# Kernel optimization log

Hardware: AMD Instinct MI355X
Metric: run time of the kernel (lower is better)

## Reference

```python
import jax, jax.numpy as jnp
import numpy as np

N_NODES = 50000


def gcn_conv(x, W, b, src, dst, ew, n_nodes):
    """PyG GCNConv: out = D^{-1/2}(A + I)D^{-1/2} (x @ W) + b, A weighted by ew.

    Self loops (weight 1) are handled analytically instead of appending edges.
    """
    h = x @ W  # [N, out]
    # degree includes self-loop weight of 1
    deg = jax.ops.segment_sum(ew, dst, num_segments=n_nodes) + 1.0  # [N]
    dinv = jnp.where(deg > 0, jax.lax.rsqrt(deg), 0.0)
    norm = dinv[src] * ew * dinv[dst]  # [E]
    # message = norm * h[src], scatter-add to dst
    agg = jax.ops.segment_sum(h[src] * norm[:, None], dst, num_segments=n_nodes)
    # self-loop contribution: dinv[i] * 1 * dinv[i] * h[i]
    agg = agg + h * (dinv * dinv)[:, None]
    return agg + b


def setup_inputs() -> dict:
    key = jax.random.key(0)
    k = jax.random.split(key, 8)
    n, e, d_in, d_h = N_NODES, 600000, 128, 128
    x = jax.random.normal(k[0], (n, d_in), dtype=jnp.float32)
    edge_index = jax.random.randint(k[1], (2, e), 0, n, dtype=jnp.int64)
    edge_attr = jax.random.uniform(k[2], (e,), dtype=jnp.float32)
    s1 = 1.0 / np.sqrt(d_in)
    s2 = 1.0 / np.sqrt(d_h)
    W1 = jax.random.uniform(k[3], (d_in, d_h), jnp.float32, -s1, s1)
    b1 = jnp.zeros((d_h,), jnp.float32)
    W2 = jax.random.uniform(k[4], (d_h, d_h), jnp.float32, -s2, s2)
    b2 = jnp.zeros((d_h,), jnp.float32)
    return {"x": x, "edge_index": edge_index, "edge_attr": edge_attr,
            "W1": W1, "b1": b1, "W2": W2, "b2": b2}


def reference(x, edge_index, edge_attr, W1, b1, W2, b2):
    src, dst = edge_index[0], edge_index[1]
    h = gcn_conv(x, W1, b1, src, dst, edge_attr, N_NODES)
    h = jax.nn.relu(h)
    # dropout is identity in eval mode (deterministic reference)
    out = gcn_conv(h, W2, b2, src, dst, edge_attr, N_NODES)
    return out
```

## Files before the change

### kernel.cpp

```cpp
#include <hip/hip_runtime.h>
#include <stdint.h>

#define D 128
#define EPB 4096
#define CSZ 128

typedef __bf16 bf16x8 __attribute__((ext_vector_type(8)));
typedef float f32x4 __attribute__((ext_vector_type(4)));

__device__ inline float bf2f(unsigned short u) {
    return __uint_as_float((unsigned)u << 16);
}
__device__ inline unsigned short f2bf(float f) {
    unsigned u = __float_as_uint(f);
    return (unsigned short)((u + 0x7FFF + ((u >> 16) & 1)) >> 16);
}

struct Params {
    const float* x; const int* ei; const float* ew;
    const float* W1; const float* b1; const float* W2; const float* b2;
    float* out;
    int N, E, C, B1n, total, gb, gb2, hb16, sb;
    unsigned short *Wt1, *Wt2;
    unsigned int* bh; int* ebase; int* bsums;
    float* dinv; int* cnt; int* rowstart;
    int2* brec; int2* erec;
    unsigned short *Hbuf, *Abuf;
};


__device__ inline void dev_prep(int which, const Params& p) {
    const float* W = (which == 0) ? p.W1 : p.W2;
    unsigned short* Wt = (which == 0) ? p.Wt1 : p.Wt2;
    for (int i = threadIdx.x; i < 2048; i += 256) {
        int nn = i >> 4;
        int kc = (i & 15) << 3;
        ushort4 o0, o1;
        o0.x = f2bf(W[(kc + 0) * 128 + nn]); o0.y = f2bf(W[(kc + 1) * 128 + nn]);
        o0.z = f2bf(W[(kc + 2) * 128 + nn]); o0.w = f2bf(W[(kc + 3) * 128 + nn]);
        o1.x = f2bf(W[(kc + 4) * 128 + nn]); o1.y = f2bf(W[(kc + 5) * 128 + nn]);
        o1.z = f2bf(W[(kc + 6) * 128 + nn]); o1.w = f2bf(W[(kc + 7) * 128 + nn]);
        *(ushort4*)(Wt + nn * 128 + kc) = o0;
        *(ushort4*)(Wt + nn * 128 + kc + 4) = o1;
    }
}

__device__ inline void dev_hist(int b, const Params& p, unsigned int* hist) {
    for (int i = threadIdx.x; i < p.C; i += 256) hist[i] = 0;
    __syncthreads();
    const int base = b * EPB + threadIdx.x;
#pragma unroll
    for (int k = 0; k < EPB / 256; ++k) {
        int e = base + k * 256;
        if (e < p.E) atomicAdd(&hist[((unsigned)p.ei[p.E + e]) >> 7], 1u);
    }
    __syncthreads();
    for (int i = threadIdx.x; i < p.C; i += 256) p.bh[(size_t)b * p.C + i] = hist[i];
}

__device__ inline void dev_scanA(int blk, const Params& p, int* tmp) {
    const int tid = threadIdx.x;
    const int i = blk * 256 + tid;
    int v = 0;
    if (i < p.total) {
        int c = i / p.B1n;
        int b = i - c * p.B1n;
        v = (int)p.bh[(size_t)b * p.C + c];
    }
    tmp[tid] = v;
    __syncthreads();
    for (int off = 1; off < 256; off <<= 1) {
        int t = (tid >= off) ? tmp[tid - off] : 0;
        __syncthreads();
        tmp[tid] += t;
        __syncthreads();
    }
    if (i < p.total) p.ebase[i] = tmp[tid] - v;
    if (tid == 255) p.bsums[blk] = tmp[255];
}

__device__ inline void block_pref(const Params& p, int* spref) {
    const int tid = threadIdx.x;
    int v = (tid < p.sb) ? p.bsums[tid] : 0;
    spref[tid] = v;
    __syncthreads();
    for (int off = 1; off < 256; off <<= 1) {
        int t = (tid >= off) ? spref[tid - off] : 0;
        __syncthreads();
        spref[tid] += t;
        __syncthreads();
    }
    int incl = spref[tid];
    __syncthreads();
    spref[tid] = incl - v;
    __syncthreads();
}

__device__ inline void dev_scat(int b, const Params& p, unsigned int* cur, const int* spref) {
    for (int i = threadIdx.x; i < p.C; i += 256) cur[i] = 0;
    __syncthreads();
    const int base = b * EPB + threadIdx.x;
#pragma unroll
    for (int k = 0; k < EPB / 256; ++k) {
        int e = base + k * 256;
        if (e < p.E) {
            int s = p.ei[e];
            unsigned d = (unsigned)p.ei[p.E + e];
            float w = p.ew[e];
            int c = d >> 7;
            unsigned r = atomicAdd(&cur[c], 1u);
            int idx = c * p.B1n + b;
            int pos = p.ebase[idx] + spref[idx >> 8] + (int)r;
            p.brec[pos] = make_int2((int)((d << 16) | (unsigned)s), __float_as_int(w));
        }
    }
}

__device__ inline void dev_cbuild(int c, const Params& p, unsigned int* a, const int* spref) {
    unsigned int* hcnt = a;
    unsigned int* hdeg = a + CSZ;
    unsigned int* lsc  = a + 2 * CSZ;
    unsigned int* curs = a + 3 * CSZ;
    const int tid = threadIdx.x;
    const int i0 = c * p.B1n;
    const int cs = p.ebase[i0] + spref[i0 >> 8];
    int ce;
    if (c + 1 < p.C) {
        const int i1 = (c + 1) * p.B1n;
        ce = p.ebase[i1] + spref[i1 >> 8];
    } else {
        ce = p.E;
    }
    if (tid < CSZ) { hcnt[tid] = 0; hdeg[tid] = 0; }
    __syncthreads();
    for (int i = cs + tid; i < ce; i += 256) {
        int2 r = p.brec[i];
        int local = (int)(((unsigned)r.x) >> 16) & (CSZ - 1);
        atomicAdd(&hcnt[local], 1u);
        atomicAdd(&hdeg[local], (unsigned)(__int_as_float(r.y) * 16777216.0f));
    }
    __syncthreads();
    if (tid < CSZ) lsc[tid] = hcnt[tid];
    __syncthreads();
    for (int off = 1; off < CSZ; off <<= 1) {
        unsigned t = (tid < CSZ && tid >= off) ? lsc[tid - off] : 0u;
        __syncthreads();
        if (tid < CSZ) lsc[tid] += t;
        __syncthreads();
    }
    if (tid < CSZ) {
        unsigned excl = lsc[tid] - hcnt[tid];
        curs[tid] = excl;
        int node = c * CSZ + tid;
        if (node < p.N) {
            p.rowstart[node] = cs + (int)excl;
            p.cnt[node] = (int)hcnt[tid];
            float deg = 1.0f + (float)hdeg[tid] * (1.0f / 16777216.0f);
            p.dinv[node] = rsqrtf(deg);
        }
    }
    __syncthreads();
    for (int i = cs + tid; i < ce; i += 256) {
        int2 r = p.brec[i];
        int local = (int)(((unsigned)r.x) >> 16) & (CSZ - 1);
        unsigned rk = atomicAdd(&curs[local], 1u);
        p.erec[cs + (int)rk] = make_int2(r.x & 0xFFFF, r.y);
    }
}

template <bool IN_BF16>
__device__ inline void mfma_body(unsigned short* sE,
                                 const void* __restrict__ Xv,
                                 const unsigned short* __restrict__ Wt,
                                 unsigned short* __restrict__ H, int n, int blk) {
    const int tid = threadIdx.x;
    const int row0 = blk * 64;
    const int lane = tid & 63;
    const int wv = tid >> 6;
    const int qm = lane & 15;
    const int quad = lane >> 4;

    const int arow = row0 + wv * 16 + qm;
    const int ar = (arow < n) ? arow : (n - 1);

    f32x4 acc[8];
#pragma unroll
    for (int i = 0; i < 8; ++i) acc[i] = (f32x4){0.f, 0.f, 0.f, 0.f};

#pragma unroll
    for (int kb = 0; kb < 4; ++kb) {
        const int koff = kb * 32 + quad * 8;
        bf16x8 a;
        if (IN_BF16) {
            a = *(const bf16x8*)((const unsigned short*)Xv + (size_t)ar * 128 + koff);
        } else {
            const float* Xf = (const float*)Xv + (size_t)ar * 128 + koff;
            float4 v0 = *(const float4*)(Xf);
            float4 v1 = *(const float4*)(Xf + 4);
            union { bf16x8 v; ushort4 u[2]; } cv;
            cv.u[0].x = f2bf(v0.x); cv.u[0].y = f2bf(v0.y);
            cv.u[0].z = f2bf(v0.z); cv.u[0].w = f2bf(v0.w);
            cv.u[1].x = f2bf(v1.x); cv.u[1].y = f2bf(v1.y);
            cv.u[1].z = f2bf(v1.z); cv.u[1].w = f2bf(v1.w);
            a = cv.v;
        }
#pragma unroll
        for (int n0 = 0; n0 < 8; ++n0) {
            bf16x8 b = *(const bf16x8*)(Wt + (n0 * 16 + qm) * 128 + koff);
            acc[n0] = __builtin_amdgcn_mfma_f32_16x16x32_bf16(a, b, acc[n0], 0, 0, 0);
        }
    }

#pragma unroll
    for (int n0 = 0; n0 < 8; ++n0)
#pragma unroll
        for (int r = 0; r < 4; ++r)
            sE[(wv * 16 + quad * 4 + r) * 136 + n0 * 16 + qm] = f2bf(acc[n0][r]);
    __syncthreads();

    const int row_in = lane >> 2;
    const int c0 = (lane & 3) * 4;
    const int grow = row0 + wv * 16 + row_in;
    if (grow < n) {
#pragma unroll
        for (int j = 0; j < 4; ++j)
            *(int4*)(H + (size_t)grow * 128 + (c0 + j) * 8) =
                *(const int4*)(&sE[(wv * 16 + row_in) * 136 + (c0 + j) * 8]);
    }
}

__device__ inline void gather1_node16(const Params& p, unsigned short* dst, int node, int lane) {
    const int4* __restrict__ H16 = (const int4*)p.Hbuf;
    union U8 { int4 v; unsigned short u[8]; };
    if (node < p.N) {
        const int start = p.rowstart[node];
        const int m = p.cnt[node];
        const float di = p.dinv[node];
        U8 s; s.v = H16[(size_t)node * 16 + lane];
        float acc[8];
#pragma unroll
        for (int q = 0; q < 8; ++q) acc[q] = di * bf2f(s.u[q]);

        const int2* __restrict__ er = p.erec + start;
        int j = 0;
        for (; j + 4 <= m; j += 4) {
            int2 e0 = er[j], e1 = er[j + 1], e2 = er[j + 2], e3 = er[j + 3];
            U8 v0, v1, v2, v3;
            v0.v = H16[(size_t)e0.x * 16 + lane];
            v1.v = H16[(size_t)e1.x * 16 + lane];
            v2.v = H16[(size_t)e2.x * 16 + lane];
            v3.v = H16[(size_t)e3.x * 16 + lane];
            float w0 = p.dinv[e0.x] * __int_as_float(e0.y);
            float w1 = p.dinv[e1.x] * __int_as_float(e1.y);
            float w2 = p.dinv[e2.x] * __int_as_float(e2.y);
            float w3 = p.dinv[e3.x] * __int_as_float(e3.y);
#pragma unroll
            for (int q = 0; q < 8; ++q)
                acc[q] += w0 * bf2f(v0.u[q]) + w1 * bf2f(v1.u[q]) +
                          w2 * bf2f(v2.u[q]) + w3 * bf2f(v3.u[q]);
        }
        for (; j < m; ++j) {
            int2 e0 = er[j];
            U8 v0; v0.v = H16[(size_t)e0.x * 16 + lane];
            float w0 = p.dinv[e0.x] * __int_as_float(e0.y);
#pragma unroll
            for (int q = 0; q < 8; ++q) acc[q] += w0 * bf2f(v0.u[q]);
        }
        const float4 b0 = *(const float4*)(p.b1 + lane * 8);
        const float4 b1v = *(const float4*)(p.b1 + lane * 8 + 4);
        const float bb[8] = {b0.x, b0.y, b0.z, b0.w, b1v.x, b1v.y, b1v.z, b1v.w};
        U8 o;
#pragma unroll
        for (int q = 0; q < 8; ++q) o.u[q] = f2bf(fmaxf(bb[q] + di * acc[q], 0.f));
        *(int4*)dst = o.v;
    } else {
        *(int4*)dst = (int4){0, 0, 0, 0};
    }
}

__device__ inline void gather2_body16(const Params& p, const int4* __restrict__ H16,
                                      const float* __restrict__ bias,
                                      float4* __restrict__ OUT, int g) {
    const int lane = threadIdx.x & 15;
    const int node = g * 16 + (threadIdx.x >> 4);
    if (node >= p.N) return;
    const int start = p.rowstart[node];
    const int m = p.cnt[node];
    const float di = p.dinv[node];

    union U8 { int4 v; unsigned short u[8]; };
    U8 s; s.v = H16[(size_t)node * 16 + lane];
    float acc[8];
#pragma unroll
    for (int q = 0; q < 8; ++q) acc[q] = bf2f(s.u[q]);

    const int2* __restrict__ er = p.erec + start;
    int j = 0;
    for (; j + 4 <= m; j += 4) {
        int2 e0 = er[j], e1 = er[j + 1], e2 = er[j + 2], e3 = er[j + 3];
        U8 v0, v1, v2, v3;
        v0.v = H16[(size_t)e0.x * 16 + lane];
        v1.v = H16[(size_t)e1.x * 16 + lane];
        v2.v = H16[(size_t)e2.x * 16 + lane];
        v3.v = H16[(size_t)e3.x * 16 + lane];
        float w0 = __int_as_float(e0.y), w1 = __int_as_float(e1.y);
        float w2 = __int_as_float(e2.y), w3 = __int_as_float(e3.y);
#pragma unroll
        for (int q = 0; q < 8; ++q)
            acc[q] += w0 * bf2f(v0.u[q]) + w1 * bf2f(v1.u[q]) +
                      w2 * bf2f(v2.u[q]) + w3 * bf2f(v3.u[q]);
    }
    for (; j < m; ++j) {
        int2 e0 = er[j];
        U8 v0; v0.v = H16[(size_t)e0.x * 16 + lane];
        float w0 = __int_as_float(e0.y);
#pragma unroll
        for (int q = 0; q < 8; ++q) acc[q] += w0 * bf2f(v0.u[q]);
    }

    const float4 b0 = *(const float4*)(bias + lane * 8);
    const float4 b1v = *(const float4*)(bias + lane * 8 + 4);
    float4 f0, f1;
    f0.x = b0.x + di * acc[0]; f0.y = b0.y + di * acc[1];
    f0.z = b0.z + di * acc[2]; f0.w = b0.w + di * acc[3];
    f1.x = b1v.x + di * acc[4]; f1.y = b1v.y + di * acc[5];
    f1.z = b1v.z + di * acc[6]; f1.w = b1v.w + di * acc[7];
    OUT[(size_t)node * 32 + lane * 2] = f0;
    OUT[(size_t)node * 32 + lane * 2 + 1] = f1;
}

__global__ __launch_bounds__(256, 4) void k_f0(Params p) {
    __shared__ __align__(16) unsigned int hist[512];
    if (blockIdx.x < 2) dev_prep(blockIdx.x, p);
    else dev_hist(blockIdx.x - 2, p, hist);
}
__global__ __launch_bounds__(256, 4) void k_f1(Params p) {
    __shared__ __align__(16) char arena[64 * 136 * 2];
    if ((int)blockIdx.x < p.gb) mfma_body<false>((unsigned short*)arena, (const void*)p.x, p.Wt1, p.Hbuf, p.N, blockIdx.x);
    else dev_scanA(blockIdx.x - p.gb, p, (int*)arena);
}
__global__ __launch_bounds__(256) void k_f3(Params p) {
    __shared__ unsigned int cur[512];
    __shared__ int spref[256];
    block_pref(p, spref);
    dev_scat(blockIdx.x, p, cur, spref);
}
__global__ __launch_bounds__(256) void k_f4(Params p) {
    __shared__ unsigned int a[4 * CSZ];
    __shared__ int spref[256];
    block_pref(p, spref);
    dev_cbuild(blockIdx.x, p, a, spref);
}
__global__ __launch_bounds__(256, 4) void k_g5(Params p) {
    __shared__ __align__(16) unsigned short sA[32 * 136];
    __shared__ __align__(16) unsigned short sE[32 * 136];
    const int row0 = blockIdx.x * 32;
    const int tid = threadIdx.x;

    const int lane16 = tid & 15;
    const int grp16 = tid >> 4;
#pragma unroll
    for (int pass = 0; pass < 2; ++pass) {
        const int local = pass * 16 + grp16;
        gather1_node16(p, sA + local * 136 + lane16 * 8, row0 + local, lane16);
    }
    __syncthreads();

    const int lane = tid & 63;
    const int wv = tid >> 6;
    const int qm = lane & 15;
    const int quad = lane >> 4;
    const int rh = wv & 1;
    const int ch = wv >> 1;

    f32x4 acc[4];
#pragma unroll
    for (int i = 0; i < 4; ++i) acc[i] = (f32x4){0.f, 0.f, 0.f, 0.f};

#pragma unroll
    for (int kb = 0; kb < 4; ++kb) {
        const int koff = kb * 32 + quad * 8;
        bf16x8 a = *(const bf16x8*)(sA + (rh * 16 + qm) * 136 + koff);
#pragma unroll
        for (int n0 = 0; n0 < 4; ++n0) {
            bf16x8 b = *(const bf16x8*)(p.Wt2 + ((ch * 4 + n0) * 16 + qm) * 128 + koff);
            acc[n0] = __builtin_amdgcn_mfma_f32_16x16x32_bf16(a, b, acc[n0], 0, 0, 0);
        }
    }

    const int crow = rh * 16 + quad * 4;
    float di[4];
#pragma unroll
    for (int r = 0; r < 4; ++r) {
        int rr = row0 + crow + r;
        int rc = (rr < p.N) ? rr : (p.N - 1);
        di[r] = p.dinv[rc];
    }

#pragma unroll
    for (int n0 = 0; n0 < 4; ++n0)
#pragma unroll
        for (int r = 0; r < 4; ++r)
            sE[(crow + r) * 136 + ch * 64 + n0 * 16 + qm] = f2bf(acc[n0][r] * di[r]);
    __syncthreads();

    const int row_in = tid >> 3;
    const int c0 = (tid & 7) * 2;
    const int grow = row0 + row_in;
    if (grow < p.N) {
        *(int4*)(p.Abuf + (size_t)grow * 128 + (c0 + 0) * 8) =
            *(const int4*)(&sE[row_in * 136 + (c0 + 0) * 8]);
        *(int4*)(p.Abuf + (size_t)grow * 128 + (c0 + 1) * 8) =
            *(const int4*)(&sE[row_in * 136 + (c0 + 1) * 8]);
    }
}
__global__ __launch_bounds__(256) void k_g6(Params p) {
    gather2_body16(p, (const int4*)p.Abuf, p.b2, (float4*)p.out, blockIdx.x);
}

extern "C" void kernel_launch(void* const* d_in, const int* in_sizes, int n_in,
                              void* d_out, int out_size, void* d_ws, size_t ws_size,
                              hipStream_t stream) {
    Params p;
    p.x  = (const float*)d_in[0];
    p.ei = (const int*)d_in[1];
    p.ew = (const float*)d_in[2];
    p.W1 = (const float*)d_in[3];
    p.b1 = (const float*)d_in[4];
    p.W2 = (const float*)d_in[5];
    p.b2 = (const float*)d_in[6];
    p.out = (float*)d_out;

    p.N = in_sizes[0] / D;
    p.E = in_sizes[2];
    p.C = (p.N + CSZ - 1) / CSZ;
    p.B1n = (p.E + EPB - 1) / EPB;
    p.total = p.C * p.B1n;
    p.sb = (p.total + 255) / 256;
    p.gb = (p.N + 63) / 64;
    p.gb2 = (p.N + 31) / 32;
    p.hb16 = (p.N + 15) / 16;

    char* w = (char*)d_ws;
    auto alloc = [&](size_t bytes) {
        void* r = (void*)w;
        w += (bytes + 255) & ~(size_t)255;
        return r;
    };
    p.bh       = (unsigned int*)alloc((size_t)p.total * 4);
    p.ebase    = (int*)alloc((size_t)p.total * 4);
    p.bsums    = (int*)alloc((size_t)(p.sb + 1) * 4);
    p.dinv     = (float*)alloc((size_t)p.N * 4);
    p.cnt      = (int*)alloc((size_t)p.N * 4);
    p.rowstart = (int*)alloc((size_t)p.N * 4);
    p.brec     = (int2*)alloc((size_t)p.E * 8);
    p.erec     = (int2*)alloc((size_t)p.E * 8);
    p.Hbuf     = (unsigned short*)alloc((size_t)p.N * D * 2);
    p.Abuf     = (unsigned short*)alloc((size_t)p.N * D * 2);
    p.Wt1      = (unsigned short*)alloc(128 * 128 * 2);
    p.Wt2      = (unsigned short*)alloc(128 * 128 * 2);

    k_f0<<<2 + p.B1n, 256, 0, stream>>>(p);
    k_f1<<<p.gb + p.sb, 256, 0, stream>>>(p);
    k_f3<<<p.B1n, 256, 0, stream>>>(p);
    k_f4<<<p.C, 256, 0, stream>>>(p);
    k_g5<<<p.gb2, 256, 0, stream>>>(p);
    k_g6<<<p.hb16, 256, 0, stream>>>(p);
}
```

Baseline: 198.8 us.

## Spread first-layer GEMM blocks across scan, scatter and CSR-build kernels

The X@W1 MFMA GEMM blocks, previously all launched alongside the scan kernel, are now split across three launches (1/8, 3/8, remaining) and co-scheduled with the scan, edge-scatter and CSR-build phases. The aim is to fill idle CUs in the small, latency-bound graph preprocessing kernels with independent dense work. It also places scan blocks first so they get scheduled early. Scatter and build kernels now use the larger shared arena and a 4-blocks-per-CU launch bound, which could change their occupancy.

```diff
diff --git a/kernel.cpp b/kernel.cpp
--- a/kernel.cpp
+++ b/kernel.cpp
@@ -20,7 +20,7 @@
     const float* x; const int* ei; const float* ew;
     const float* W1; const float* b1; const float* W2; const float* b2;
     float* out;
-    int N, E, C, B1n, total, gb, gb2, hb16, sb;
+    int N, E, C, B1n, total, gb, gb2, hb16, sb, g1, g2, g3;
     unsigned short *Wt1, *Wt2;
     unsigned int* bh; int* ebase; int* bsums;
     float* dinv; int* cnt; int* rowstart;
@@ -336,20 +336,32 @@
 }
 __global__ __launch_bounds__(256, 4) void k_f1(Params p) {
     __shared__ __align__(16) char arena[64 * 136 * 2];
-    if ((int)blockIdx.x < p.gb) mfma_body<false>((unsigned short*)arena, (const void*)p.x, p.Wt1, p.Hbuf, p.N, blockIdx.x);
-    else dev_scanA(blockIdx.x - p.gb, p, (int*)arena);
-}
-__global__ __launch_bounds__(256) void k_f3(Params p) {
-    __shared__ unsigned int cur[512];
-    __shared__ int spref[256];
-    block_pref(p, spref);
-    dev_scat(blockIdx.x, p, cur, spref);
-}
-__global__ __launch_bounds__(256) void k_f4(Params p) {
-    __shared__ unsigned int a[4 * CSZ];
-    __shared__ int spref[256];
-    block_pref(p, spref);
-    dev_cbuild(blockIdx.x, p, a, spref);
+    if ((int)blockIdx.x < p.sb) dev_scanA(blockIdx.x, p, (int*)arena);
+    else mfma_body<false>((unsigned short*)arena, (const void*)p.x, p.Wt1, p.Hbuf, p.N, blockIdx.x - p.sb);
+}
+__global__ __launch_bounds__(256, 4) void k_f3(Params p) {
+    __shared__ __align__(16) char arena[64 * 136 * 2];
+    if ((int)blockIdx.x < p.B1n) {
+        unsigned int* cur = (unsigned int*)arena;
+        int* spref = (int*)(arena + 2048);
+        block_pref(p, spref);
+        dev_scat(blockIdx.x, p, cur, spref);
+    } else {
+        mfma_body<false>((unsigned short*)arena, (const void*)p.x, p.Wt1, p.Hbuf, p.N,
+                         p.g1 + (int)blockIdx.x - p.B1n);
+    }
+}
+__global__ __launch_bounds__(256, 4) void k_f4(Params p) {
+    __shared__ __align__(16) char arena[64 * 136 * 2];
+    if ((int)blockIdx.x < p.C) {
+        unsigned int* a = (unsigned int*)arena;
+        int* spref = (int*)(arena + 2048);
+        block_pref(p, spref);
+        dev_cbuild(blockIdx.x, p, a, spref);
+    } else {
+        mfma_body<false>((unsigned short*)arena, (const void*)p.x, p.Wt1, p.Hbuf, p.N,
+                         p.g1 + p.g2 + (int)blockIdx.x - p.C);
+    }
 }
 __global__ __launch_bounds__(256, 4) void k_g5(Params p) {
     __shared__ __align__(16) unsigned short sA[32 * 136];
@@ -440,6 +452,9 @@
     p.gb = (p.N + 63) / 64;
     p.gb2 = (p.N + 31) / 32;
     p.hb16 = (p.N + 15) / 16;
+    p.g1 = p.gb / 8;
+    p.g2 = (3 * p.gb) / 8;
+    p.g3 = p.gb - p.g1 - p.g2;
 
     char* w = (char*)d_ws;
     auto alloc = [&](size_t bytes) {
@@ -461,9 +476,9 @@
     p.Wt2      = (unsigned short*)alloc(128 * 128 * 2);
 
     k_f0<<<2 + p.B1n, 256, 0, stream>>>(p);
-    k_f1<<<p.gb + p.sb, 256, 0, stream>>>(p);
-    k_f3<<<p.B1n, 256, 0, stream>>>(p);
-    k_f4<<<p.C, 256, 0, stream>>>(p);
+    k_f1<<<p.sb + p.g1, 256, 0, stream>>>(p);
+    k_f3<<<p.B1n + p.g2, 256, 0, stream>>>(p);
+    k_f4<<<p.C + p.g3, 256, 0, stream>>>(p);
     k_g5<<<p.gb2, 256, 0, stream>>>(p);
     k_g6<<<p.hb16, 256, 0, stream>>>(p);
 }
```

Measured after the change: 194.6 us. 1.02x faster.
